# Optimization experiments

Hardware: AMD Instinct MI355X
Metric: run time of the kernel (lower is better)

The kernel has to match this reference:

```python
import jax, jax.numpy as jnp
import numpy as np

HEADS = 64
HEAD_DIM = 4
C = 256
T = 32  # num_ds_tokens
MAX_Q_CHUNK = 256


def conv1x1(x, W, b):
    # x: (N,C,H,W), W: (O,C), b: (O,)
    return jnp.einsum('oc,nchw->nohw', W, x) + b[None, :, None, None]


def reshape_heads(x):
    n, c, h, w = x.shape
    return x.reshape(n, HEADS, HEAD_DIM, h * w)


def chunked_attention(q, k, v, ds_token_count, chunk):
    # q: (N,h,d,L); k,v: (N,h,d,M)
    N, H, D, L = q.shape
    scale = 1.0 / float(np.sqrt(D))
    nc = L // chunk
    qs = q.reshape(N, H, D, nc, chunk).transpose(3, 0, 1, 2, 4)  # (nc,N,h,d,chunk)

    def body(carry, qc):
        logits = jnp.einsum('nhdl,nhdm->nhlm', qc, k) * scale
        w = jax.nn.softmax(logits, axis=-1)
        out = jnp.einsum('nhlm,nhdm->nhdl', w, v)
        total = jnp.clip(w.sum(axis=-1, keepdims=True), 1e-6, None)
        dsr = w[..., -ds_token_count:].sum(axis=-1, keepdims=True) / total  # (N,h,chunk,1)
        return carry, (out, dsr)

    _, (outs, dsrs) = jax.lax.scan(body, None, qs)
    attn_out = outs.transpose(1, 2, 3, 0, 4).reshape(N, H, D, L)
    ds_ratio_mean = dsrs.mean(axis=(0, 2, 3, 4))  # mean over heads, tokens -> (N,)
    return attn_out, ds_ratio_mean


def forward(spatials, invs, dss, Wq, bq, Wk, bk, Wv, bv, Wo, bo, Wdsk, bdsk, Wdsv, bdsv, ds_gate):
    fused_feats = []
    ds_ratios = []
    for i in range(4):
        sp, inv, ds = spatials[i], invs[i], dss[i]
        N, c, Hh, Ww = sp.shape
        q = reshape_heads(conv1x1(sp, Wq[i], bq[i]))
        k_sp = reshape_heads(conv1x1(inv, Wk[i], bk[i]))
        v_sp = reshape_heads(conv1x1(inv, Wv[i], bv[i]))
        pooled = ds.mean(axis=(2, 3))  # (N,C)
        key_tok = (pooled @ Wdsk[i].T + bdsk[i]).reshape(N, HEADS, HEAD_DIM, T)
        val_tok = (pooled @ Wdsv[i].T + bdsv[i]).reshape(N, HEADS, HEAD_DIM, T)
        gate = jax.nn.sigmoid(ds_gate[i])
        val_tok = val_tok * gate
        k = jnp.concatenate([k_sp, key_tok], axis=-1)
        v = jnp.concatenate([v_sp, val_tok], axis=-1)
        L = Hh * Ww
        chunk = min(MAX_Q_CHUNK, L)
        attn_out, dsr = chunked_attention(q, k, v, T, chunk)
        attn_out = attn_out.reshape(N, C, Hh, Ww)
        fused = sp + conv1x1(attn_out, Wo[i], bo[i])
        fused_feats.append(fused)
        ds_ratios.append(dsr)
    return (*fused_feats, jnp.stack(ds_ratios))


def setup_inputs() -> dict:
    key = jax.random.key(0)
    ks = jax.random.split(key, 32)
    sizes = [64, 32, 16, 8]
    inp = {}
    j = 0
    for pref in ('s', 'i', 'd'):
        for lvl, hw in enumerate(sizes):
            inp[f'{pref}{lvl}'] = jax.random.normal(ks[j], (2, C, hw, hw), dtype=jnp.float32)
            j += 1
    w = 0.02
    inp['Wq'] = jax.random.normal(ks[j], (4, C, C), dtype=jnp.float32) * w; j += 1
    inp['bq'] = jnp.zeros((4, C), dtype=jnp.float32)
    inp['Wk'] = jax.random.normal(ks[j], (4, C, C), dtype=jnp.float32) * w; j += 1
    inp['bk'] = jnp.zeros((4, C), dtype=jnp.float32)
    inp['Wv'] = jax.random.normal(ks[j], (4, C, C), dtype=jnp.float32) * w; j += 1
    inp['bv'] = jnp.zeros((4, C), dtype=jnp.float32)
    inp['Wo'] = jax.random.normal(ks[j], (4, C, C), dtype=jnp.float32) * w; j += 1
    inp['bo'] = jnp.zeros((4, C), dtype=jnp.float32)
    inp['Wdsk'] = jax.random.normal(ks[j], (4, HEADS * HEAD_DIM * T, C), dtype=jnp.float32) * w; j += 1
    inp['bdsk'] = jnp.zeros((4, HEADS * HEAD_DIM * T), dtype=jnp.float32)
    inp['Wdsv'] = jax.random.normal(ks[j], (4, HEADS * HEAD_DIM * T, C), dtype=jnp.float32) * w; j += 1
    inp['bdsv'] = jnp.zeros((4, HEADS * HEAD_DIM * T), dtype=jnp.float32)
    inp['ds_gate'] = jnp.zeros((4,), dtype=jnp.float32)
    return inp


def reference(s0, s1, s2, s3, i0, i1, i2, i3, d0, d1, d2, d3,
              Wq, bq, Wk, bk, Wv, bv, Wo, bo, Wdsk, bdsk, Wdsv, bdsv, ds_gate):
    return forward((s0, s1, s2, s3), (i0, i1, i2, i3), (d0, d1, d2, d3),
                   Wq, bq, Wk, bk, Wv, bv, Wo, bo, Wdsk, bdsk, Wdsv, bdsv, ds_gate)
```

## Files before the change

kernel.cpp:

```cpp
#include <hip/hip_runtime.h>
#include <math.h>

#define CCH 256
#define NB 2
#define HEADS 64
#define QK_SCALE (0.72134752f * 1024.0f)
#define SCH_MAGIC 15316.0f

typedef _Float16 f16;
typedef _Float16 f16x8 __attribute__((ext_vector_type(8)));
typedef _Float16 f16x4 __attribute__((ext_vector_type(4)));
typedef float f32x4 __attribute__((ext_vector_type(4)));

static const size_t OFF_POOLED = 0;
static const size_t OFF_DSACC  = 2048;
static const size_t H_Q   = 0;
static const size_t H_K   = 2785280;
static const size_t H_V   = 5636096;
static const size_t H_ATT = 8486912;
static const size_t H_SPT = 11272192;
static const size_t H_IVT = 14057472;
static const size_t H_W   = 16842752;

static const size_t DS_OUT_OFF = 2785280;

__device__ __forceinline__ void lvl_tables(int lvl, int& L, int& M, size_t& qo, size_t& kvo) {
    const int Ls[4] = {4096, 1024, 256, 64};
    const size_t qoff[4] = {0, 2097152, 2621440, 2752512};
    const size_t kvoff[4] = {0, 2113536, 2654208, 2801664};
    L = Ls[lvl]; M = L + 32; qo = qoff[lvl]; kvo = kvoff[lvl];
}

struct P12 { const float* a[12]; };

__global__ __launch_bounds__(256)
void prep_kernel(P12 ptrs, const float* __restrict__ Wq, const float* __restrict__ Wk,
                 const float* __restrict__ Wv, const float* __restrict__ Wo,
                 f16* __restrict__ WF, f16* __restrict__ spT, f16* __restrict__ ivT,
                 float* __restrict__ pooled, float* __restrict__ dsacc) {
    int id = blockIdx.x;
    if (id < 5440) {
        __shared__ float tile[32][33];
        int x = id % 170, rest = id / 170;
        int y = rest & 7, z = rest >> 3;
        int lvl, xl;
        if (x < 128) { lvl = 0; xl = x; }
        else if (x < 160) { lvl = 1; xl = x - 128; }
        else if (x < 168) { lvl = 2; xl = x - 160; }
        else { lvl = 3; xl = x - 168; }
        int L, M; size_t qo, kvo;
        lvl_tables(lvl, L, M, qo, kvo);
        int src = z >> 1, n = z & 1;
        const float* X = ptrs.a[src * 4 + lvl];
        f16* XT = (src == 0 ? spT : ivT) + qo;
        int c0 = y * 32, l0 = xl * 32;
        int tx = threadIdx.x & 31, ty = threadIdx.x >> 5;
        #pragma unroll
        for (int k = 0; k < 4; k++) {
            int c = c0 + ty + k * 8;
            tile[ty + k * 8][tx] = X[((size_t)n * CCH + c) * L + l0 + tx];
        }
        __syncthreads();
        #pragma unroll
        for (int k = 0; k < 4; k++) {
            int l = l0 + ty + k * 8;
            XT[((size_t)n * L + l) * CCH + c0 + tx] = (f16)tile[tx][ty + k * 8];
        }
    } else if (id < 6464) {
        int wI = id - 5440;
        int x = wI & 255, setId = wI >> 8;
        const float* src = (setId == 0) ? Wq : (setId == 1) ? Wk : (setId == 2) ? Wv : Wo;
        size_t i = ((size_t)x * 256 + threadIdx.x) * 4;
        float4 v = *(const float4*)(src + i);
        f16x4 o;
        o[0] = (f16)v.x; o[1] = (f16)v.y; o[2] = (f16)v.z; o[3] = (f16)v.w;
        *(f16x4*)(WF + (size_t)setId * 262144 + i) = o;
    } else {
        if (id == 6464) {
            dsacc[threadIdx.x] = 0.f;
            dsacc[threadIdx.x + 256] = 0.f;
        }
        int lin = (id - 6464) * 4 + (threadIdx.x >> 6);
        int c = lin & 255, n = (lin >> 8) & 1, lvl = lin >> 9;
        int t = threadIdx.x & 63;
        const float* d = ptrs.a[8 + lvl];
        int L = 4096 >> (2 * lvl);
        const float* p = d + ((size_t)n * CCH + c) * L;
        float s = 0.f;
        for (int i = t; i < L; i += 64) s += p[i];
        #pragma unroll
        for (int off = 32; off > 0; off >>= 1) s += __shfl_down(s, off);
        if (t == 0) pooled[(lvl * NB + n) * CCH + c] = s / (float)L;
    }
}

__global__ __launch_bounds__(256)
void mid_kernel(const f16* __restrict__ spT, const f16* __restrict__ ivT,
                const f16* __restrict__ WF,
                const float* __restrict__ bq, const float* __restrict__ bk,
                const float* __restrict__ bv,
                f16* __restrict__ qF, f16* __restrict__ kF, f16* __restrict__ vF,
                const float* __restrict__ Wdsk, const float* __restrict__ bdsk,
                const float* __restrict__ Wdsv, const float* __restrict__ bdsv,
                const float* __restrict__ ds_gate, const float* __restrict__ pooled) {
    int id = blockIdx.x;
    if (id >= 1032) {
        int dI = id - 1032;
        int bx = dI & 63, lvl = dI >> 6;
        int t = threadIdx.x;
        int j = bx * 128 + (t >> 1);
        int half = t & 1;
        const float4* wk = (const float4*)(Wdsk + ((size_t)lvl * 8192 + j) * CCH) + half * 32;
        const float4* wv = (const float4*)(Wdsv + ((size_t)lvl * 8192 + j) * CCH) + half * 32;
        const float4* p0 = (const float4*)(pooled + (size_t)(lvl * NB + 0) * CCH) + half * 32;
        const float4* p1 = (const float4*)(pooled + (size_t)(lvl * NB + 1) * CCH) + half * 32;
        float ak0 = 0.f, ak1 = 0.f, av0 = 0.f, av1 = 0.f;
        #pragma unroll 8
        for (int c4 = 0; c4 < 32; c4++) {
            float4 a = wk[c4], b = wv[c4], pa = p0[c4], pb = p1[c4];
            ak0 += a.x * pa.x + a.y * pa.y + a.z * pa.z + a.w * pa.w;
            ak1 += a.x * pb.x + a.y * pb.y + a.z * pb.z + a.w * pb.w;
            av0 += b.x * pa.x + b.y * pa.y + b.z * pa.z + b.w * pa.w;
            av1 += b.x * pb.x + b.y * pb.y + b.z * pb.z + b.w * pb.w;
        }
        ak0 += __shfl_xor(ak0, 1); ak1 += __shfl_xor(ak1, 1);
        av0 += __shfl_xor(av0, 1); av1 += __shfl_xor(av1, 1);
        if (half) return;
        float bk_ = bdsk[lvl * 8192 + j], bv_ = bdsv[lvl * 8192 + j];
        float gate = 1.f / (1.f + __expf(-ds_gate[lvl]));
        ak0 += bk_; ak1 += bk_;
        av0 = (av0 + bv_) * gate; av1 = (av1 + bv_) * gate;
        int o = j >> 5, tk = j & 31;
        int L, M; size_t qo, kvo;
        lvl_tables(lvl, L, M, qo, kvo);
        kF[kvo + ((size_t)(0 * M + L + tk)) * CCH + o] = (f16)ak0;
        kF[kvo + ((size_t)(1 * M + L + tk)) * CCH + o] = (f16)ak1;
        vF[kvo + ((size_t)(0 * CCH + o)) * M + L + tk] = (f16)av0;
        vF[kvo + ((size_t)(1 * CCH + o)) * M + L + tk] = (f16)av1;
        return;
    }
    int x = id % 43, rest = id / 43;
    int yb = rest % 12, n = rest / 12;
    int lvl, xl;
    if (x < 32) { lvl = 0; xl = x; }
    else if (x < 40) { lvl = 1; xl = x - 32; }
    else if (x < 42) { lvl = 2; xl = x - 40; }
    else { lvl = 3; xl = x - 42; }
    int L, M; size_t qo, kvo;
    lvl_tables(lvl, L, M, qo, kvo);
    const int type = yb >> 2;
    const int ob = (yb & 3) * 64;
    const int t = threadIdx.x, w = t >> 6, lane = t & 63;
    const int quad = lane >> 4, n16 = lane & 15;
    const int l0w = xl * 128 + w * 32;
    if (l0w >= L) return;

    const f16* XT = ((type == 0) ? spT : ivT) + qo;
    const f16* Wf = WF + (size_t)type * 262144 + (size_t)lvl * 65536;
    const float* bias = ((type == 0) ? bq : (type == 1) ? bk : bv) + lvl * 256;

    f32x4 acc[4][2];
    #pragma unroll
    for (int f = 0; f < 4; f++)
        #pragma unroll
        for (int g = 0; g < 2; g++) { acc[f][g][0]=0.f; acc[f][g][1]=0.f; acc[f][g][2]=0.f; acc[f][g][3]=0.f; }

    const f16* xp = XT + ((size_t)n * L + l0w + n16) * CCH + quad * 8;
    const f16* wp = Wf + ((size_t)(ob + n16)) * CCH + quad * 8;

    #pragma unroll
    for (int c0 = 0; c0 < 256; c0 += 32) {
        f16x8 af[4], bf[2];
        #pragma unroll
        for (int f = 0; f < 4; f++) af[f] = *(const f16x8*)(wp + (size_t)f * 16 * CCH + c0);
        #pragma unroll
        for (int g = 0; g < 2; g++) bf[g] = *(const f16x8*)(xp + (size_t)g * 16 * CCH + c0);
        #pragma unroll
        for (int f = 0; f < 4; f++)
            #pragma unroll
            for (int g = 0; g < 2; g++)
                acc[f][g] = __builtin_amdgcn_mfma_f32_16x16x32_f16(af[f], bf[g], acc[f][g], 0, 0, 0);
    }

    #pragma unroll
    for (int f = 0; f < 4; f++) {
        #pragma unroll
        for (int g = 0; g < 2; g++) {
            int lloc = l0w + g * 16 + n16;
            float vals[4];
            #pragma unroll
            for (int r = 0; r < 4; r++)
                vals[r] = acc[f][g][r] + bias[ob + f * 16 + quad * 4 + r];
            if (type == 0) {
                #pragma unroll
                for (int r = 0; r < 4; r++)
                    qF[qo + ((size_t)n * CCH + ob + f * 16 + quad * 4 + r) * (size_t)L + lloc] =
                        (f16)(vals[r] * QK_SCALE);
            } else if (type == 1) {
                f16x4 pk;
                #pragma unroll
                for (int r = 0; r < 4; r++) pk[r] = (f16)vals[r];
                *(f16x4*)(kF + kvo + ((size_t)n * M + lloc) * CCH + ob + f * 16 + quad * 4) = pk;
            } else {
                #pragma unroll
                for (int r = 0; r < 4; r++)
                    vF[kvo + ((size_t)n * CCH + ob + f * 16 + quad * 4 + r) * (size_t)M + lloc] =
                        (f16)vals[r];
            }
        }
    }
}

__global__ __launch_bounds__(256)
void attn_all_kernel(const f16* __restrict__ qBase, const f16* __restrict__ kBase,
                     const f16* __restrict__ vBase, f16* __restrict__ attBase,
                     float* __restrict__ dsacc) {
    int x = blockIdx.x, lvl, xl;
    if (x < 8) { lvl = 0; xl = x; }
    else if (x < 10) { lvl = 1; xl = x - 8; }
    else if (x < 11) { lvl = 2; xl = x - 10; }
    else { lvl = 3; xl = x - 11; }
    int L, M; size_t qo, kvo;
    lvl_tables(lvl, L, M, qo, kvo);
    const f16* qb = qBase + qo;
    const f16* kT = kBase + kvo;
    const f16* vb = vBase + kvo;
    f16* attT = attBase + qo;

    const int h = blockIdx.y, b = blockIdx.z;
    const int t = threadIdx.x, w = t >> 6, lane = t & 63;
    const int quad = lane >> 4, n16 = lane & 15;
    const size_t qbase = ((size_t)b * CCH + h * 4) * (size_t)L;
    const int mperm = ((n16 & 12) << 1) + (n16 & 3);
    const int base_tile = xl * 32;

    f16x4 qf[8];
    f32x4 acc[8];
    #pragma unroll
    for (int i = 0; i < 8; i++) {
        #pragma unroll
        for (int e = 0; e < 4; e++) qf[i][e] = (f16)0.f;
        acc[i][0] = 0.f; acc[i][1] = 0.f; acc[i][2] = 0.f; acc[i][3] = 0.f;
    }

    const f16* kp = kT + ((size_t)b * M + mperm) * CCH + h * 4;
    const f16* vp = vb + ((size_t)b * CCH + h * 4 + (n16 & 3)) * (size_t)M + quad * 8;
    const bool vlane = (n16 < 4);

    f32x4 magic;
    magic[0] = SCH_MAGIC; magic[1] = SCH_MAGIC; magic[2] = SCH_MAGIC; magic[3] = SCH_MAGIC;

    f16x8 vcon0, vconL;
    {
        f16 c0 = (f16)((n16 == 4) ? 1.f : 0.f);
        f16 cL = (f16)((n16 == 4 || n16 == 5) ? 1.f : 0.f);
        #pragma unroll
        for (int e = 0; e < 8; e++) { vcon0[e] = c0; vconL[e] = cL; }
    }

#define ATTN_CHUNK(m0_, vcon_)                                                          \
    do {                                                                                \
        f16x4 ka = *(const f16x4*)(kp + (size_t)(m0_) * CCH);                           \
        f16x4 kb2 = *(const f16x4*)(kp + (size_t)(m0_) * CCH + 4 * CCH);                \
        f16x8 vf = vlane ? *(const f16x8*)(vp + (m0_)) : (vcon_);                       \
        _Pragma("unroll")                                                               \
        for (int g = 0; g < 2; g++) {                                                   \
            f32x4 s[4][2];                                                              \
            _Pragma("unroll")                                                           \
            for (int j = 0; j < 4; j++) {                                               \
                s[j][0] = __builtin_amdgcn_mfma_f32_16x16x16f16(ka, qf[g*4+j], magic, 0, 0, 0);  \
                s[j][1] = __builtin_amdgcn_mfma_f32_16x16x16f16(kb2, qf[g*4+j], magic, 0, 0, 0); \
            }                                                                           \
            _Pragma("unroll")                                                           \
            for (int j = 0; j < 4; j++) {                                               \
                union { unsigned u[4]; f16x8 hh; } Wu;                                  \
                Wu.u[0] = ((unsigned)(int)s[j][0][0]) | (((unsigned)(int)s[j][0][1]) << 16); \
                Wu.u[1] = ((unsigned)(int)s[j][0][2]) | (((unsigned)(int)s[j][0][3]) << 16); \
                Wu.u[2] = ((unsigned)(int)s[j][1][0]) | (((unsigned)(int)s[j][1][1]) << 16); \
                Wu.u[3] = ((unsigned)(int)s[j][1][2]) | (((unsigned)(int)s[j][1][3]) << 16); \
                acc[g*4+j] = __builtin_amdgcn_mfma_f32_16x16x32_f16(Wu.hh, vf, acc[g*4+j], 0, 0, 0); \
            }                                                                           \
        }                                                                               \
    } while (0)

    if (base_tile * 16 + 512 <= L) {
        if (quad == 0) {
            #pragma unroll
            for (int i = 0; i < 8; i++) {
                int l = (base_tile + i * 4 + w) * 16 + n16;
                #pragma unroll
                for (int d = 0; d < 4; d++) qf[i][d] = qb[qbase + (size_t)d * L + l];
            }
        }
        for (int m0 = 0; m0 < L; m0 += 64) {
            ATTN_CHUNK(m0, vcon0);
            ATTN_CHUNK(m0 + 32, vcon0);
        }
        ATTN_CHUNK(L, vconL);
    } else {
        bool valid[8];
        #pragma unroll
        for (int i = 0; i < 8; i++) {
            int tl0 = (base_tile + i * 4 + w) * 16;
            valid[i] = (tl0 < L);
            if (valid[i] && quad == 0) {
                int l = tl0 + n16;
                #pragma unroll
                for (int d = 0; d < 4; d++) qf[i][d] = qb[qbase + (size_t)d * L + l];
            }
        }
        for (int m0 = 0; m0 < M; m0 += 32) {
            f16x4 ka = *(const f16x4*)(kp + (size_t)m0 * CCH);
            f16x4 kb2 = *(const f16x4*)(kp + (size_t)m0 * CCH + 4 * CCH);
            f16x8 vf = vlane ? *(const f16x8*)(vp + m0) : ((m0 >= L) ? vconL : vcon0);
            #pragma unroll
            for (int g = 0; g < 2; g++) {
                f32x4 s[4][2];
                #pragma unroll
                for (int j = 0; j < 4; j++) {
                    if (!valid[g * 4 + j]) continue;
                    s[j][0] = __builtin_amdgcn_mfma_f32_16x16x16f16(ka, qf[g*4+j], magic, 0, 0, 0);
                    s[j][1] = __builtin_amdgcn_mfma_f32_16x16x16f16(kb2, qf[g*4+j], magic, 0, 0, 0);
                }
                #pragma unroll
                for (int j = 0; j < 4; j++) {
                    if (!valid[g * 4 + j]) continue;
                    union { unsigned u[4]; f16x8 hh; } Wu;
                    Wu.u[0] = ((unsigned)(int)s[j][0][0]) | (((unsigned)(int)s[j][0][1]) << 16);
                    Wu.u[1] = ((unsigned)(int)s[j][0][2]) | (((unsigned)(int)s[j][0][3]) << 16);
                    Wu.u[2] = ((unsigned)(int)s[j][1][0]) | (((unsigned)(int)s[j][1][1]) << 16);
                    Wu.u[3] = ((unsigned)(int)s[j][1][2]) | (((unsigned)(int)s[j][1][3]) << 16);
                    acc[g*4+j] = __builtin_amdgcn_mfma_f32_16x16x32_f16(Wu.hh, vf, acc[g*4+j], 0, 0, 0);
                }
            }
        }
    }
#undef ATTN_CHUNK

    float dsr = 0.f;
    #pragma unroll
    for (int i = 0; i < 8; i++) {
        int tl0 = (base_tile + i * 4 + w) * 16;
        if (tl0 >= L) continue;
        #pragma unroll
        for (int r = 0; r < 4; r++) {
            float den = __shfl(acc[i][r], (lane & 48) | 4, 64);
            float rcp = 1.f / den;
            int l = tl0 + quad * 4 + r;
            if (n16 < 4)
                attT[((size_t)b * L + l) * CCH + h * 4 + n16] = (f16)(acc[i][r] * rcp);
            if (n16 == 5) dsr += acc[i][r] * rcp;
        }
    }
    dsr += __shfl_xor(dsr, 16, 64);
    dsr += __shfl_xor(dsr, 32, 64);
    if (n16 == 5 && quad == 0) atomicAdd(dsacc + (size_t)lvl * 128 + (size_t)b * 64 + h, dsr);
}

__global__ __launch_bounds__(256)
void convo_kernel(const f16* __restrict__ attT, const f16* __restrict__ WF,
                  const float* __restrict__ bo, const float* __restrict__ s0,
                  const float* __restrict__ s1, const float* __restrict__ s2,
                  const float* __restrict__ s3, float* __restrict__ out,
                  const float* __restrict__ dsacc) {
    if (blockIdx.x == 0 && blockIdx.y == 0 && blockIdx.z == 0 && threadIdx.x < 64) {
        int tt = threadIdx.x;
        #pragma unroll
        for (int i = 0; i < 8; i++) {
            float v = dsacc[i * 64 + tt];
            #pragma unroll
            for (int off = 32; off > 0; off >>= 1) v += __shfl_down(v, off);
            if (tt == 0) {
                int lv = i >> 1;
                out[DS_OUT_OFF + i] = v / (float)(HEADS * (4096 >> (2 * lv)));
            }
        }
    }
    int x = blockIdx.x, lvl, xl;
    if (x < 32) { lvl = 0; xl = x; }
    else if (x < 40) { lvl = 1; xl = x - 32; }
    else if (x < 42) { lvl = 2; xl = x - 40; }
    else { lvl = 3; xl = x - 42; }
    int L, M; size_t qo, kvo;
    lvl_tables(lvl, L, M, qo, kvo);
    const float* resid = (lvl == 0) ? s0 : (lvl == 1) ? s1 : (lvl == 2) ? s2 : s3;
    const int ob = blockIdx.y * 64;
    const int n = blockIdx.z;
    const int t = threadIdx.x, w = t >> 6, lane = t & 63;
    const int quad = lane >> 4, n16 = lane & 15;
    const int l0w = xl * 128 + w * 32;
    if (l0w >= L) return;

    const f16* Wf = WF + 3 * 262144 + (size_t)lvl * 65536;
    const float* bias = bo + lvl * 256;

    f32x4 acc[4][2];
    #pragma unroll
    for (int f = 0; f < 4; f++)
        #pragma unroll
        for (int g = 0; g < 2; g++) { acc[f][g][0]=0.f; acc[f][g][1]=0.f; acc[f][g][2]=0.f; acc[f][g][3]=0.f; }

    const f16* xp = attT + qo + ((size_t)n * L + l0w + n16) * CCH + quad * 8;
    const f16* wp = Wf + ((size_t)(ob + n16)) * CCH + quad * 8;

    #pragma unroll
    for (int c0 = 0; c0 < 256; c0 += 32) {
        f16x8 af[4], bf[2];
        #pragma unroll
        for (int f = 0; f < 4; f++) af[f] = *(const f16x8*)(wp + (size_t)f * 16 * CCH + c0);
        #pragma unroll
        for (int g = 0; g < 2; g++) bf[g] = *(const f16x8*)(xp + (size_t)g * 16 * CCH + c0);
        #pragma unroll
        for (int f = 0; f < 4; f++)
            #pragma unroll
            for (int g = 0; g < 2; g++)
                acc[f][g] = __builtin_amdgcn_mfma_f32_16x16x32_f16(af[f], bf[g], acc[f][g], 0, 0, 0);
    }

    #pragma unroll
    for (int f = 0; f < 4; f++) {
        #pragma unroll
        for (int g = 0; g < 2; g++) {
            int lloc = l0w + g * 16 + n16;
            #pragma unroll
            for (int r = 0; r < 4; r++) {
                size_t idx = qo + ((size_t)n * CCH + ob + f * 16 + quad * 4 + r) * (size_t)L + lloc;
                out[idx] = acc[f][g][r] + bias[ob + f * 16 + quad * 4 + r] + resid[idx - qo];
            }
        }
    }
}

extern "C" void kernel_launch(void* const* d_in, const int* in_sizes, int n_in,
                              void* d_out, int out_size, void* d_ws, size_t ws_size,
                              hipStream_t stream) {
    const float* sp[4] = {(const float*)d_in[0], (const float*)d_in[1], (const float*)d_in[2], (const float*)d_in[3]};
    const float* iv[4] = {(const float*)d_in[4], (const float*)d_in[5], (const float*)d_in[6], (const float*)d_in[7]};
    const float* dd[4] = {(const float*)d_in[8], (const float*)d_in[9], (const float*)d_in[10], (const float*)d_in[11]};
    const float* Wq = (const float*)d_in[12];
    const float* bq = (const float*)d_in[13];
    const float* Wk = (const float*)d_in[14];
    const float* bk = (const float*)d_in[15];
    const float* Wv = (const float*)d_in[16];
    const float* bv = (const float*)d_in[17];
    const float* Wo = (const float*)d_in[18];
    const float* bo = (const float*)d_in[19];
    const float* Wdsk = (const float*)d_in[20];
    const float* bdsk = (const float*)d_in[21];
    const float* Wdsv = (const float*)d_in[22];
    const float* bdsv = (const float*)d_in[23];
    const float* gate = (const float*)d_in[24];

    float* ws = (float*)d_ws;
    float* pooled = ws + OFF_POOLED;
    float* dsacc = ws + OFF_DSACC;
    f16* hb = (f16*)((char*)d_ws + 10240);
    f16* qF   = hb + H_Q;
    f16* kF   = hb + H_K;
    f16* vF   = hb + H_V;
    f16* attF = hb + H_ATT;
    f16* spT  = hb + H_SPT;
    f16* ivT  = hb + H_IVT;
    f16* WF   = hb + H_W;
    float* out = (float*)d_out;

    P12 ptrs;
    for (int i = 0; i < 4; i++) { ptrs.a[i] = sp[i]; ptrs.a[4 + i] = iv[i]; ptrs.a[8 + i] = dd[i]; }

    prep_kernel<<<dim3(6976), 256, 0, stream>>>(ptrs, Wq, Wk, Wv, Wo, WF, spT, ivT, pooled, dsacc);

    mid_kernel<<<dim3(1288), 256, 0, stream>>>(spT, ivT, WF, bq, bk, bv, qF, kF, vF,
                                               Wdsk, bdsk, Wdsv, bdsv, gate, pooled);

    attn_all_kernel<<<dim3(12, 64, 2), 256, 0, stream>>>(qF, kF, vF, attF, dsacc);

    convo_kernel<<<dim3(43, 4, 2), 256, 0, stream>>>(attF, WF, bo, sp[0], sp[1], sp[2], sp[3],
                                                     out, dsacc);
}
```

Measured before the change: 571.8 us.

## Stage K/V tiles through double-buffered LDS in attention main loop

The full-tile attention path now cooperatively loads 128-key chunks of K and V into double-buffered shared memory. The next chunk is prefetched into registers while MFMAs run on the current one, and LDS constant rows supply the ones/zero V rows. This replaces per-lane global loads, some redundant, with shared LDS reads so memory latency overlaps compute. In exchange it adds a __syncthreads per chunk and assumes L is a multiple of 256, since the loop steps c by 2.

```diff
diff --git a/kernel.cpp b/kernel.cpp
--- a/kernel.cpp
+++ b/kernel.cpp
@@ -227,6 +227,9 @@
     const f16* vb = vBase + kvo;
     f16* attT = attBase + qo;
 
+    __shared__ __align__(16) f16 Klds[2][128][4];
+    __shared__ __align__(16) f16 Vlds[2][16][136];
+
     const int h = blockIdx.y, b = blockIdx.z;
     const int t = threadIdx.x, w = t >> 6, lane = t & 63;
     const int quad = lane >> 4, n16 = lane & 15;
@@ -283,6 +286,47 @@
         }                                                                               \
     } while (0)
 
+#define ATTN_SUB(cur_, sub_)                                                            \
+    do {                                                                                \
+        f16x4 ka = *(const f16x4*)(kAddr + (cur_) * 512 + (sub_) * 128);                \
+        f16x4 kb2 = *(const f16x4*)(kAddr + (cur_) * 512 + (sub_) * 128 + 16);          \
+        f16x8 vf = *(const f16x8*)(vAddr + (cur_) * 2176 + (sub_) * 32);                \
+        _Pragma("unroll")                                                               \
+        for (int g = 0; g < 2; g++) {                                                   \
+            f32x4 s[4][2];                                                              \
+            _Pragma("unroll")                                                           \
+            for (int j = 0; j < 4; j++) {                                               \
+                s[j][0] = __builtin_amdgcn_mfma_f32_16x16x16f16(ka, qf[g*4+j], magic, 0, 0, 0);  \
+                s[j][1] = __builtin_amdgcn_mfma_f32_16x16x16f16(kb2, qf[g*4+j], magic, 0, 0, 0); \
+            }                                                                           \
+            _Pragma("unroll")                                                           \
+            for (int j = 0; j < 4; j++) {                                               \
+                union { unsigned u[4]; f16x8 hh; } Wu;                                  \
+                Wu.u[0] = ((unsigned)(int)s[j][0][0]) | (((unsigned)(int)s[j][0][1]) << 16); \
+                Wu.u[1] = ((unsigned)(int)s[j][0][2]) | (((unsigned)(int)s[j][0][3]) << 16); \
+                Wu.u[2] = ((unsigned)(int)s[j][1][0]) | (((unsigned)(int)s[j][1][1]) << 16); \
+                Wu.u[3] = ((unsigned)(int)s[j][1][2]) | (((unsigned)(int)s[j][1][3]) << 16); \
+                acc[g*4+j] = __builtin_amdgcn_mfma_f32_16x16x32_f16(Wu.hh, vf, acc[g*4+j], 0, 0, 0); \
+            }                                                                           \
+        }                                                                               \
+    } while (0)
+
+#define PIPE_ITER(c_, cur_)                                                             \
+    {                                                                                   \
+        unsigned kvr = 0, vvr = 0;                                                      \
+        const bool nxt_ = ((c_) + 1 < nch);                                             \
+        if (nxt_) {                                                                     \
+            kvr = *(const unsigned*)(kgsrc + (size_t)((c_) + 1) * (128 * CCH));         \
+            vvr = *(const unsigned*)(vgsrc + ((c_) + 1) * 128);                         \
+        }                                                                               \
+        ATTN_SUB(cur_, 0); ATTN_SUB(cur_, 1); ATTN_SUB(cur_, 2); ATTN_SUB(cur_, 3);     \
+        if (nxt_) {                                                                     \
+            *(unsigned*)(kdst + (1 - (cur_)) * 512) = kvr;                              \
+            *(unsigned*)(vdst + (1 - (cur_)) * 2176) = vvr;                             \
+        }                                                                               \
+        __syncthreads();                                                                \
+    }
+
     if (base_tile * 16 + 512 <= L) {
         if (quad == 0) {
             #pragma unroll
@@ -292,9 +336,25 @@
                 for (int d = 0; d < 4; d++) qf[i][d] = qb[qbase + (size_t)d * L + l];
             }
         }
-        for (int m0 = 0; m0 < L; m0 += 64) {
-            ATTN_CHUNK(m0, vcon0);
-            ATTN_CHUNK(m0 + 32, vcon0);
+        const f16* kgsrc = kT + ((size_t)b * M + w * 32 + (lane >> 1)) * CCH + h * 4 + (lane & 1) * 2;
+        const f16* vgsrc = vb + ((size_t)b * CCH + h * 4 + w) * (size_t)M + lane * 2;
+        f16* kdst = &Klds[0][w * 32 + (lane >> 1)][(lane & 1) * 2];
+        f16* vdst = &Vlds[0][w][lane * 2];
+
+        for (int i = t; i < 2 * 12 * 68; i += 256) {
+            int buf = i / 816, r = i % 816;
+            *(unsigned*)&Vlds[buf][4 + r / 68][(r % 68) * 2] = ((r / 68) == 0) ? 0x3C003C00u : 0u;
+        }
+        *(unsigned*)kdst = *(const unsigned*)kgsrc;
+        *(unsigned*)vdst = *(const unsigned*)vgsrc;
+        __syncthreads();
+
+        const f16* kAddr = &Klds[0][0][0] + mperm * 4;
+        const f16* vAddr = &Vlds[0][0][0] + n16 * 136 + quad * 8;
+        const int nch = L >> 7;
+        for (int c = 0; c < nch; c += 2) {
+            PIPE_ITER(c, 0);
+            PIPE_ITER(c + 1, 1);
         }
         ATTN_CHUNK(L, vconL);
     } else {
@@ -336,6 +396,8 @@
         }
     }
 #undef ATTN_CHUNK
+#undef ATTN_SUB
+#undef PIPE_ITER
 
     float dsr = 0.f;
     #pragma unroll
```

Result: faster. 540.9 us (-5.4%).

## Store K/V head-major per batch and prefetch next K/V chunk in attention

Applied to the files above, without the earlier changes.

The projection kernel and the DS-token kernel now write K and V in a per-(batch, head) contiguous layout of 4×M elements, instead of a channel-strided layout. In the old layout each lane's 8-byte K read sat 512 bytes from its neighbour's. The attention kernel reads from this layout, so the K/V loads for one head come from one compact region. The fast path also software-pipelines the K/V register loads, fetching the next 32-key chunk before computing the current one to hide global load latency. The cost is a few extra live registers and unconditional V loads on lanes that later replace the value with constants.

```diff
diff --git a/kernel.cpp b/kernel.cpp
--- a/kernel.cpp
+++ b/kernel.cpp
@@ -133,10 +133,11 @@
         int o = j >> 5, tk = j & 31;
         int L, M; size_t qo, kvo;
         lvl_tables(lvl, L, M, qo, kvo);
-        kF[kvo + ((size_t)(0 * M + L + tk)) * CCH + o] = (f16)ak0;
-        kF[kvo + ((size_t)(1 * M + L + tk)) * CCH + o] = (f16)ak1;
-        vF[kvo + ((size_t)(0 * CCH + o)) * M + L + tk] = (f16)av0;
-        vF[kvo + ((size_t)(1 * CCH + o)) * M + L + tk] = (f16)av1;
+        int hh = o >> 2, dd = o & 3;
+        kF[kvo + ((size_t)(0 * 64 + hh)) * (4 * (size_t)M) + (size_t)(L + tk) * 4 + dd] = (f16)ak0;
+        kF[kvo + ((size_t)(1 * 64 + hh)) * (4 * (size_t)M) + (size_t)(L + tk) * 4 + dd] = (f16)ak1;
+        vF[kvo + ((size_t)(0 * 64 + hh)) * (4 * (size_t)M) + (size_t)dd * M + (L + tk)] = (f16)av0;
+        vF[kvo + ((size_t)(1 * 64 + hh)) * (4 * (size_t)M) + (size_t)dd * M + (L + tk)] = (f16)av1;
         return;
     }
     int x = id % 43, rest = id / 43;
@@ -200,12 +201,14 @@
                 f16x4 pk;
                 #pragma unroll
                 for (int r = 0; r < 4; r++) pk[r] = (f16)vals[r];
-                *(f16x4*)(kF + kvo + ((size_t)n * M + lloc) * CCH + ob + f * 16 + quad * 4) = pk;
+                int hh = (ob + f * 16 + quad * 4) >> 2;
+                *(f16x4*)(kF + kvo + ((size_t)(n * 64 + hh)) * (4 * (size_t)M) + (size_t)lloc * 4) = pk;
             } else {
+                int hh = (ob + f * 16 + quad * 4) >> 2;
+                f16* vdst = vF + kvo + ((size_t)(n * 64 + hh)) * (4 * (size_t)M) + lloc;
                 #pragma unroll
                 for (int r = 0; r < 4; r++)
-                    vF[kvo + ((size_t)n * CCH + ob + f * 16 + quad * 4 + r) * (size_t)M + lloc] =
-                        (f16)vals[r];
+                    vdst[(size_t)r * M] = (f16)vals[r];
             }
         }
     }
@@ -223,8 +226,6 @@
     int L, M; size_t qo, kvo;
     lvl_tables(lvl, L, M, qo, kvo);
     const f16* qb = qBase + qo;
-    const f16* kT = kBase + kvo;
-    const f16* vb = vBase + kvo;
     f16* attT = attBase + qo;
 
     const int h = blockIdx.y, b = blockIdx.z;
@@ -234,6 +235,12 @@
     const int mperm = ((n16 & 12) << 1) + (n16 & 3);
     const int base_tile = xl * 32;
 
+    const f16* kh = kBase + kvo + ((size_t)(b * 64 + h)) * (4 * (size_t)M);
+    const f16* vh = vBase + kvo + ((size_t)(b * 64 + h)) * (4 * (size_t)M);
+    const f16* kpm = kh + (size_t)mperm * 4;
+    const f16* vpm = vh + (size_t)(n16 & 3) * M + quad * 8;
+    const bool vlane = (n16 < 4);
+
     f16x4 qf[8];
     f32x4 acc[8];
     #pragma unroll
@@ -242,10 +249,6 @@
         for (int e = 0; e < 4; e++) qf[i][e] = (f16)0.f;
         acc[i][0] = 0.f; acc[i][1] = 0.f; acc[i][2] = 0.f; acc[i][3] = 0.f;
     }
-
-    const f16* kp = kT + ((size_t)b * M + mperm) * CCH + h * 4;
-    const f16* vp = vb + ((size_t)b * CCH + h * 4 + (n16 & 3)) * (size_t)M + quad * 8;
-    const bool vlane = (n16 < 4);
 
     f32x4 magic;
     magic[0] = SCH_MAGIC; magic[1] = SCH_MAGIC; magic[2] = SCH_MAGIC; magic[3] = SCH_MAGIC;
@@ -258,18 +261,23 @@
         for (int e = 0; e < 8; e++) { vcon0[e] = c0; vconL[e] = cL; }
     }
 
-#define ATTN_CHUNK(m0_, vcon_)                                                          \
+#define LOADKV(m0_, ka_, kb_, vf_)                                                      \
     do {                                                                                \
-        f16x4 ka = *(const f16x4*)(kp + (size_t)(m0_) * CCH);                           \
-        f16x4 kb2 = *(const f16x4*)(kp + (size_t)(m0_) * CCH + 4 * CCH);                \
-        f16x8 vf = vlane ? *(const f16x8*)(vp + (m0_)) : (vcon_);                       \
+        ka_ = *(const f16x4*)(kpm + (size_t)(m0_) * 4);                                 \
+        kb_ = *(const f16x4*)(kpm + (size_t)(m0_) * 4 + 16);                            \
+        vf_ = *(const f16x8*)(vpm + (m0_));                                             \
+    } while (0)
+
+#define COMPUTE32(ka_, kb_, vfl_, vcon_)                                                \
+    do {                                                                                \
+        f16x8 vf = vlane ? (vfl_) : (vcon_);                                            \
         _Pragma("unroll")                                                               \
         for (int g = 0; g < 2; g++) {                                                   \
             f32x4 s[4][2];                                                              \
             _Pragma("unroll")                                                           \
             for (int j = 0; j < 4; j++) {                                               \
-                s[j][0] = __builtin_amdgcn_mfma_f32_16x16x16f16(ka, qf[g*4+j], magic, 0, 0, 0);  \
-                s[j][1] = __builtin_amdgcn_mfma_f32_16x16x16f16(kb2, qf[g*4+j], magic, 0, 0, 0); \
+                s[j][0] = __builtin_amdgcn_mfma_f32_16x16x16f16((ka_), qf[g*4+j], magic, 0, 0, 0);  \
+                s[j][1] = __builtin_amdgcn_mfma_f32_16x16x16f16((kb_), qf[g*4+j], magic, 0, 0, 0); \
             }                                                                           \
             _Pragma("unroll")                                                           \
             for (int j = 0; j < 4; j++) {                                               \
@@ -292,11 +300,16 @@
                 for (int d = 0; d < 4; d++) qf[i][d] = qb[qbase + (size_t)d * L + l];
             }
         }
+        f16x4 kaA, kbA, kaB, kbB;
+        f16x8 vA, vB;
+        LOADKV(0, kaA, kbA, vA);
         for (int m0 = 0; m0 < L; m0 += 64) {
-            ATTN_CHUNK(m0, vcon0);
-            ATTN_CHUNK(m0 + 32, vcon0);
-        }
-        ATTN_CHUNK(L, vconL);
+            LOADKV(m0 + 32, kaB, kbB, vB);
+            COMPUTE32(kaA, kbA, vA, vcon0);
+            LOADKV(m0 + 64, kaA, kbA, vA);
+            COMPUTE32(kaB, kbB, vB, vcon0);
+        }
+        COMPUTE32(kaA, kbA, vA, vconL);
     } else {
         bool valid[8];
         #pragma unroll
@@ -310,9 +323,10 @@
             }
         }
         for (int m0 = 0; m0 < M; m0 += 32) {
-            f16x4 ka = *(const f16x4*)(kp + (size_t)m0 * CCH);
-            f16x4 kb2 = *(const f16x4*)(kp + (size_t)m0 * CCH + 4 * CCH);
-            f16x8 vf = vlane ? *(const f16x8*)(vp + m0) : ((m0 >= L) ? vconL : vcon0);
+            f16x4 ka = *(const f16x4*)(kpm + (size_t)m0 * 4);
+            f16x4 kb2 = *(const f16x4*)(kpm + (size_t)m0 * 4 + 16);
+            f16x8 vfl = *(const f16x8*)(vpm + m0);
+            f16x8 vf = vlane ? vfl : ((m0 >= L) ? vconL : vcon0);
             #pragma unroll
             for (int g = 0; g < 2; g++) {
                 f32x4 s[4][2];
@@ -335,7 +349,8 @@
             }
         }
     }
-#undef ATTN_CHUNK
+#undef LOADKV
+#undef COMPUTE32
 
     float dsr = 0.f;
     #pragma unroll
```

New measurement: 563.2 us. No clear change (-1.5%).
